# Optimization experiments

Hardware: AMD Instinct MI355X
Metric: run time of the kernel (lower is better)

The kernel has to match this reference:

```python
import math
import jax, jax.numpy as jnp
import numpy as np

ROPE_DIMS = 16  # rope applied to last 16 channels only
N_WIN = 16      # sliding window size


def rmsnorm(x, w):
    return x * jax.lax.rsqrt(jnp.mean(x * x, axis=-1, keepdims=True) + 1e-8) * w


def apply_rope(x, negate=False):
    # x: [B, H, T, C]; rotate last ROPE_DIMS channels with interleaved pairs
    T = x.shape[2]
    x_pass, x_rope = x[..., :-ROPE_DIMS], x[..., -ROPE_DIMS:]
    t = jnp.arange(T, dtype=x.dtype)
    if negate:
        t = -t
    k = jnp.arange(ROPE_DIMS // 2, dtype=x.dtype)
    theta = 10000.0 ** (-2.0 * k / ROPE_DIMS)          # [8]
    freqs = t[:, None] * theta[None, :]                 # [T, 8]
    cos, sin = jnp.cos(freqs), jnp.sin(freqs)
    x1, x2 = x_rope[..., 0::2], x_rope[..., 1::2]
    rx1 = x1 * cos - x2 * sin
    rx2 = x1 * sin + x2 * cos
    rx = jnp.stack([rx1, rx2], axis=-1).reshape(x_rope.shape)
    return jnp.concatenate([x_pass, rx], axis=-1)


def setup_inputs() -> dict:
    key = jax.random.key(0)
    ks = jax.random.split(key, 14)
    B, T, d, c, nh = 4, 2048, 256, 64, 4
    s = 0.02
    return {
        "H": jax.random.normal(ks[0], (B, T, d), jnp.float32),
        "W_Q": jax.random.normal(ks[1], (nh * c, d), jnp.float32) * s,
        "W_K": jax.random.normal(ks[2], (c, d), jnp.float32) * s,
        "W_V": jax.random.normal(ks[3], (c, d), jnp.float32) * s,
        "wq": 1.0 + 0.1 * jax.random.normal(ks[4], (nh, c), jnp.float32),
        "wk": 1.0 + 0.1 * jax.random.normal(ks[5], (c,), jnp.float32),
        "wv": 1.0 + 0.1 * jax.random.normal(ks[6], (c,), jnp.float32),
        "Wg0": jax.random.normal(ks[7], (64, 2 * c), jnp.float32) * s,
        "bg0": jnp.zeros((64,), jnp.float32),
        "Wg1": jax.random.normal(ks[8], (64, 2 * c), jnp.float32) * s,
        "bg1": jnp.zeros((64,), jnp.float32),
        "Wout": jax.random.normal(ks[9], (d, 128), jnp.float32) * s,
        "bout": jnp.zeros((d,), jnp.float32),
    }


def reference(H, W_Q, W_K, W_V, wq, wk, wv, Wg0, bg0, Wg1, bg1, Wout, bout):
    B, T, d = H.shape
    nh, c = wq.shape
    # projections
    Q = (H @ W_Q.T).reshape(B, T, nh, c).transpose(0, 2, 1, 3)   # [B,nh,T,c]
    K = (H @ W_K.T)[:, None]                                      # [B,1,T,c]
    V = (H @ W_V.T)[:, None]                                      # [B,1,T,c]
    # per-head RMSNorm on Q, shared RMSNorm on K/V
    Q = rmsnorm(Q, wq[None, :, None, :])
    K = rmsnorm(K, wk)
    V = rmsnorm(V, wv)
    # partial RoPE (last 16 dims); V is also rotated in this module
    Q = apply_rope(Q)
    K = apply_rope(K)[:, 0]                                       # [B,T,c]
    V = apply_rope(V)[:, 0]
    # dense scores with sliding-window causal mask (width N_WIN)
    S = jnp.einsum('bhtc,bsc->bhts', Q, K) / math.sqrt(c)
    i = jnp.arange(T)[:, None]
    j = jnp.arange(T)[None, :]
    allowed = (j <= i) & (j >= i - (N_WIN - 1))                   # [T,T]
    S = jnp.where(allowed, S, -jnp.inf)
    P = jax.nn.softmax(S, axis=-1)
    O = jnp.einsum('bhts,bsc->bhtc', P, V)                        # [B,nh,T,c]
    O = apply_rope(O, negate=True)
    # group heads {0,1} and {2,3}
    O_g0 = O[:, :2].transpose(0, 2, 1, 3).reshape(B, T, 2 * c)
    O_g1 = O[:, 2:].transpose(0, 2, 1, 3).reshape(B, T, 2 * c)
    p0 = O_g0 @ Wg0.T + bg0
    p1 = O_g1 @ Wg1.T + bg1
    p_all = jnp.concatenate([p0, p1], axis=-1)                    # [B,T,128]
    return p_all @ Wout.T + bout
```

## Files before the change

kernel.cpp:

```cpp
#include <hip/hip_runtime.h>
#include <math.h>

#define T_SEQ 2048
#define DMODEL 256
#define C_HEAD 64
#define NH 4
#define NWIN 16
#define B_SZ 4

typedef __attribute__((ext_vector_type(8))) short bf16x8;
typedef __attribute__((ext_vector_type(8))) unsigned short ushort8;
typedef __attribute__((ext_vector_type(4))) float f32x4;

#define BAR() asm volatile("s_waitcnt lgkmcnt(0)\n\ts_barrier" ::: "memory")

static __device__ __forceinline__ unsigned short f2bf(float f) {
    union { float f; unsigned int u; } v; v.f = f;
    unsigned int r = v.u + 0x7FFFu + ((v.u >> 16) & 1u);
    return (unsigned short)(r >> 16);
}

__global__ __launch_bounds__(256) void conv_w_kernel(
    const float* __restrict__ WQ, const float* __restrict__ WK,
    const float* __restrict__ WV, const float* __restrict__ Wg0,
    const float* __restrict__ Wg1, const float* __restrict__ Wout,
    unsigned short* __restrict__ dst, float2* __restrict__ rtab) {
    const int tid = threadIdx.x;
    if (blockIdx.x >= 72) {
        const int idx = (blockIdx.x - 72) * 256 + tid;
        const int t = idx >> 3, k = idx & 7;
        const float theta = powf(10000.0f, -0.125f * (float)k);
        const float fr = (float)t * theta;
        rtab[idx] = make_float2(cosf(fr), sinf(fr));
        return;
    }
    const int i = blockIdx.x * 256 + tid;
    const float* s; long off; long doff;
    if (i < 12288) {
        const long e = (long)i * 8;
        const int col = (int)(e >> 8), k = (int)(e & 255);
        if      (col < 256) { s = WQ; off = (long)col * 256 + k; }
        else if (col < 320) { s = WK; off = (long)(col - 256) * 256 + k; }
        else                { s = WV; off = (long)(col - 320) * 256 + k; }
        doff = ((long)(col >> 4) * 8 + (k >> 5)) * 512 + ((k >> 3) & 3) * 128 + (col & 15) * 8;
    } else {
        const long e = (long)(i - 12288) * 8;
        const int col = (int)(e >> 7), k = (int)(e & 127);
        if      (col < 64)  { s = Wg0; off = (long)col * 128 + k; }
        else if (col < 128) { s = Wg1; off = (long)(col - 64) * 128 + k; }
        else                { s = Wout; off = (long)(col - 128) * 128 + k; }
        doff = 98304 + ((long)(col >> 4) * 4 + (k >> 5)) * 512 + ((k >> 3) & 3) * 128 + (col & 15) * 8;
    }
    const float4* s4 = (const float4*)(s + off);
    float4 a = s4[0], b = s4[1];
    ushort8 o;
    o[0] = f2bf(a.x); o[1] = f2bf(a.y); o[2] = f2bf(a.z); o[3] = f2bf(a.w);
    o[4] = f2bf(b.x); o[5] = f2bf(b.y); o[6] = f2bf(b.z); o[7] = f2bf(b.w);
    *(ushort8*)(dst + doff) = o;
}

__global__ __launch_bounds__(512) void fused_kernel(
    const float* __restrict__ H, const unsigned short* __restrict__ Wallb,
    const float* __restrict__ wq, const float* __restrict__ wk,
    const float* __restrict__ wv, const float2* __restrict__ rtab,
    const float* __restrict__ bg0, const float* __restrict__ bg1,
    const float* __restrict__ bout, float* __restrict__ out)
{
    __shared__ __align__(16) char smem[37888];
    char* lds_a = smem;
    char* o_lds = smem;
    char* p_lds = smem + 8192;
    char* q_lds = smem + 16384;
    char* k_lds = smem + 24576;
    char* v_t   = smem + 28672;
    char* p_att = smem + 33792;

    const int tid = threadIdx.x;
    const int blk = blockIdx.x;
    const int b  = blk >> 7;
    const int t0 = (blk & 127) << 4;

    const unsigned short* Wpk2 = Wallb + 98304;

    const int w  = tid >> 6;
    const int l  = tid & 63;
    const int g  = l >> 4;
    const int li = l & 15;
    const int lane16 = l * 8;

    const int cb0  = (w < 4) ? (w * 4) : (16 + ((w - 4) >> 1) * 4);
    const int rowa = (w < 4) ? (16 + li) : (((w - 4) & 1) * 16 + li);
    const int sel  = (w - 4) >> 1;
    const int mfh  = (w - 4) & 1;

#define WFRAG(nf, ks) (*(const bf16x8*)(Wallb + (size_t)((cb0 + (nf)) * 8 + (ks)) * 512 + lane16))

    for (int idx = tid; idx < 1024; idx += 512) {
        int row = idx >> 5, ch = idx & 31;
        int t = t0 - 16 + row; if (t < 0) t = 0;
        const float4* s4 = (const float4*)(H + ((size_t)b * T_SEQ + t) * DMODEL + ch * 8);
        float4 a = s4[0], c = s4[1];
        ushort8 o;
        o[0] = f2bf(a.x); o[1] = f2bf(a.y); o[2] = f2bf(a.z); o[3] = f2bf(a.w);
        o[4] = f2bf(c.x); o[5] = f2bf(c.y); o[6] = f2bf(c.z); o[7] = f2bf(c.w);
        int byte = row * 512 + ch * 16;
        byte ^= (row & 7) << 4;
        *(ushort8*)(lds_a + byte) = o;
    }
    bf16x8 cur[4], nxt[4];
    #pragma unroll
    for (int nf = 0; nf < 4; ++nf) { cur[nf] = WFRAG(nf, 0); nxt[nf] = WFRAG(nf, 1); }
    BAR();

    f32x4 acc[4] = {};
    #pragma unroll
    for (int ks = 0; ks < 8; ++ks) {
        bf16x8 fut[4];
        if (ks < 6) {
            #pragma unroll
            for (int nf = 0; nf < 4; ++nf) fut[nf] = WFRAG(nf, ks + 2);
        }
        int abyte = rowa * 512 + (ks * 32 + g * 8) * 2;
        abyte ^= (rowa & 7) << 4;
        bf16x8 a = *(const bf16x8*)(lds_a + abyte);
        #pragma unroll
        for (int nf = 0; nf < 4; ++nf)
            acc[nf] = __builtin_amdgcn_mfma_f32_16x16x32_bf16(a, cur[nf], acc[nf], 0, 0, 0);
        #pragma unroll
        for (int nf = 0; nf < 4; ++nf) { cur[nf] = nxt[nf]; nxt[nf] = fut[nf]; }
    }

    if (w < 4) {
        float gw[4];
        #pragma unroll
        for (int nf = 0; nf < 4; ++nf) gw[nf] = wq[w * 64 + nf * 16 + li];
        #pragma unroll
        for (int r = 0; r < 4; ++r) {
            float x0 = acc[0][r], x1 = acc[1][r];
            float x2 = acc[2][r], x3 = acc[3][r];
            float ss = x0 * x0 + x1 * x1 + x2 * x2 + x3 * x3;
            ss += __shfl_xor(ss, 1);
            ss += __shfl_xor(ss, 2);
            ss += __shfl_xor(ss, 4);
            ss += __shfl_xor(ss, 8);
            const float rinv = rsqrtf(ss * (1.0f / 64.0f) + 1e-8f);
            const int tok = g * 4 + r;
            const int t = t0 + tok;
            float v0 = x0 * rinv * gw[0];
            float v1 = x1 * rinv * gw[1];
            float v2 = x2 * rinv * gw[2];
            float v3 = x3 * rinv * gw[3];
            float2 cs = rtab[t * 8 + (li >> 1)];
            float px = __shfl_xor(v3, 1);
            v3 = ((li & 1) == 0) ? (v3 * cs.x - px * cs.y) : (px * cs.y + v3 * cs.x);
            char* qb = q_lds + w * 2048;
            const int sw = (tok & 7) << 4;
            *(unsigned short*)(qb + ((tok * 128 + (0 * 16 + li) * 2) ^ sw)) = f2bf(v0);
            *(unsigned short*)(qb + ((tok * 128 + (1 * 16 + li) * 2) ^ sw)) = f2bf(v1);
            *(unsigned short*)(qb + ((tok * 128 + (2 * 16 + li) * 2) ^ sw)) = f2bf(v2);
            *(unsigned short*)(qb + ((tok * 128 + (3 * 16 + li) * 2) ^ sw)) = f2bf(v3);
        }
    } else {
        float gw[4];
        #pragma unroll
        for (int nf = 0; nf < 4; ++nf)
            gw[nf] = (sel == 0) ? wk[nf * 16 + li] : wv[nf * 16 + li];
        #pragma unroll
        for (int r = 0; r < 4; ++r) {
            float x0 = acc[0][r], x1 = acc[1][r];
            float x2 = acc[2][r], x3 = acc[3][r];
            float ss = x0 * x0 + x1 * x1 + x2 * x2 + x3 * x3;
            ss += __shfl_xor(ss, 1);
            ss += __shfl_xor(ss, 2);
            ss += __shfl_xor(ss, 4);
            ss += __shfl_xor(ss, 8);
            const float rinv = rsqrtf(ss * (1.0f / 64.0f) + 1e-8f);
            const int row = mfh * 16 + g * 4 + r;
            int tk = t0 - 16 + row; if (tk < 0) tk = 0;
            float v0 = x0 * rinv * gw[0];
            float v1 = x1 * rinv * gw[1];
            float v2 = x2 * rinv * gw[2];
            float v3 = x3 * rinv * gw[3];
            float2 cs = rtab[tk * 8 + (li >> 1)];
            float px = __shfl_xor(v3, 1);
            v3 = ((li & 1) == 0) ? (v3 * cs.x - px * cs.y) : (px * cs.y + v3 * cs.x);
            if (sel == 0) {
                const int sw = (row & 7) << 4;
                *(unsigned short*)(k_lds + ((row * 128 + (0 * 16 + li) * 2) ^ sw)) = f2bf(v0);
                *(unsigned short*)(k_lds + ((row * 128 + (1 * 16 + li) * 2) ^ sw)) = f2bf(v1);
                *(unsigned short*)(k_lds + ((row * 128 + (2 * 16 + li) * 2) ^ sw)) = f2bf(v2);
                *(unsigned short*)(k_lds + ((row * 128 + (3 * 16 + li) * 2) ^ sw)) = f2bf(v3);
            } else {
                *(unsigned short*)(v_t + (0 * 16 + li) * 80 + row * 2) = f2bf(v0);
                *(unsigned short*)(v_t + (1 * 16 + li) * 80 + row * 2) = f2bf(v1);
                *(unsigned short*)(v_t + (2 * 16 + li) * 80 + row * 2) = f2bf(v2);
                *(unsigned short*)(v_t + (3 * 16 + li) * 80 + row * 2) = f2bf(v3);
            }
        }
    }
    BAR();

    const int gate = w >> 2, colq = w & 3;
    bf16x8 gpre[4];
    if (w >= 4) {
        #pragma unroll
        for (int ks = 0; ks < 4; ++ks)
            gpre[ks] = *(const bf16x8*)(Wpk2 + (size_t)((gate * 4 + colq) * 4 + ks) * 512 + lane16);
    }
    if (w < 4) {
        const int h = w;
        bf16x8 qf0, qf1;
        {
            const char* qb = q_lds + h * 2048;
            const int sw = (li & 7) << 4;
            qf0 = *(const bf16x8*)(qb + ((li * 128 + g * 16) ^ sw));
            qf1 = *(const bf16x8*)(qb + ((li * 128 + 64 + g * 16) ^ sw));
        }
        f32x4 st[2];
        #pragma unroll
        for (int tile = 0; tile < 2; ++tile) {
            const int row = tile * 16 + li;
            const int sw = (row & 7) << 4;
            bf16x8 kf0 = *(const bf16x8*)(k_lds + ((row * 128 + g * 16) ^ sw));
            bf16x8 kf1 = *(const bf16x8*)(k_lds + ((row * 128 + 64 + g * 16) ^ sw));
            f32x4 sa = {};
            sa = __builtin_amdgcn_mfma_f32_16x16x32_bf16(kf0, qf0, sa, 0, 0, 0);
            sa = __builtin_amdgcn_mfma_f32_16x16x32_bf16(kf1, qf1, sa, 0, 0, 0);
            st[tile] = sa;
        }

        float p[8];
        float mx = -1e30f;
        #pragma unroll
        for (int tile = 0; tile < 2; ++tile) {
            #pragma unroll
            for (int r = 0; r < 4; ++r) {
                int krel = tile * 16 - 16 + g * 4 + r;
                int dd = li - krel;
                bool ok = ((unsigned)dd < 16u) && (t0 + krel >= 0);
                float v = ok ? st[tile][r] * 0.125f : -1e30f;
                p[tile * 4 + r] = v;
                mx = fmaxf(mx, v);
            }
        }
        mx = fmaxf(mx, __shfl_xor(mx, 16));
        mx = fmaxf(mx, __shfl_xor(mx, 32));
        float sum = 0.f;
        #pragma unroll
        for (int i = 0; i < 8; ++i) { p[i] = __expf(p[i] - mx); sum += p[i]; }
        sum += __shfl_xor(sum, 16);
        sum += __shfl_xor(sum, 32);
        const float inv = 1.0f / sum;

        bf16x8 paf;
        {
            char* pbase = p_att + h * 1024;
            uint2 w0, w1;
            w0.x = (unsigned)f2bf(p[0] * inv) | ((unsigned)f2bf(p[1] * inv) << 16);
            w0.y = (unsigned)f2bf(p[2] * inv) | ((unsigned)f2bf(p[3] * inv) << 16);
            w1.x = (unsigned)f2bf(p[4] * inv) | ((unsigned)f2bf(p[5] * inv) << 16);
            w1.y = (unsigned)f2bf(p[6] * inv) | ((unsigned)f2bf(p[7] * inv) << 16);
            const int sw = (li & 3) << 4;
            *(uint2*)(pbase + ((li * 64 + 0 * 32 + g * 8) ^ sw)) = w0;
            *(uint2*)(pbase + ((li * 64 + 1 * 32 + g * 8) ^ sw)) = w1;
            asm volatile("s_waitcnt lgkmcnt(0)" ::: "memory");
            paf = *(const bf16x8*)(pbase + ((li * 64 + g * 16) ^ sw));
        }

        f32x4 o[4] = {};
        #pragma unroll
        for (int ctile = 0; ctile < 4; ++ctile) {
            bf16x8 vf = *(const bf16x8*)(v_t + (ctile * 16 + li) * 80 + g * 16);
            o[ctile] = __builtin_amdgcn_mfma_f32_16x16x32_bf16(paf, vf, o[ctile], 0, 0, 0);
        }

        #pragma unroll
        for (int r = 0; r < 4; ++r) {
            const int row = g * 4 + r;
            const int t = t0 + row;
            float o3 = o[3][r];
            float po = __shfl_xor(o3, 1);
            float2 cs = rtab[t * 8 + (li >> 1)];
            o3 = ((li & 1) == 0) ? (o3 * cs.x + po * cs.y) : (-po * cs.y + o3 * cs.x);
            #pragma unroll
            for (int ctile = 0; ctile < 4; ++ctile) {
                const int col = h * 64 + ctile * 16 + li;
                int byte = row * 512 + col * 2;
                byte ^= (row & 7) << 4;
                float val = (ctile == 3) ? o3 : o[ctile][r];
                *(unsigned short*)(o_lds + byte) = f2bf(val);
            }
        }
        #pragma unroll
        for (int ks = 0; ks < 4; ++ks)
            gpre[ks] = *(const bf16x8*)(Wpk2 + (size_t)((gate * 4 + colq) * 4 + ks) * 512 + lane16);
    }
    BAR();

    bf16x8 opre[2][4];
    {
        const float* bg = gate ? bg1 : bg0;
        f32x4 accp = {};
        #pragma unroll
        for (int ks = 0; ks < 4; ++ks) {
            int byte = li * 512 + (gate * 128 + ks * 32 + g * 8) * 2;
            byte ^= (li & 7) << 4;
            bf16x8 a = *(const bf16x8*)(o_lds + byte);
            accp = __builtin_amdgcn_mfma_f32_16x16x32_bf16(a, gpre[ks], accp, 0, 0, 0);
        }
        #pragma unroll
        for (int nf = 0; nf < 2; ++nf)
            #pragma unroll
            for (int ks = 0; ks < 4; ++ks)
                opre[nf][ks] = *(const bf16x8*)(Wpk2 + (size_t)((8 + w * 2 + nf) * 4 + ks) * 512 + lane16);
        const int cl = colq * 16 + li;
        const int pcol = gate * 64 + cl;
        const float bb = bg[cl];
        #pragma unroll
        for (int r = 0; r < 4; ++r) {
            const int row = g * 4 + r;
            int byte = row * 256 + pcol * 2;
            byte ^= (row & 7) << 4;
            *(unsigned short*)(p_lds + byte) = f2bf(accp[r] + bb);
        }
    }
    BAR();

    {
        f32x4 acco[2] = {};
        #pragma unroll
        for (int ks = 0; ks < 4; ++ks) {
            int byte = li * 256 + (ks * 32 + g * 8) * 2;
            byte ^= (li & 7) << 4;
            bf16x8 a = *(const bf16x8*)(p_lds + byte);
            #pragma unroll
            for (int nf = 0; nf < 2; ++nf)
                acco[nf] = __builtin_amdgcn_mfma_f32_16x16x32_bf16(a, opre[nf][ks], acco[nf], 0, 0, 0);
        }
        #pragma unroll
        for (int nf = 0; nf < 2; ++nf) {
            const int col = w * 32 + nf * 16 + li;
            const float bb = bout[col];
            #pragma unroll
            for (int r = 0; r < 4; ++r) {
                const int row = g * 4 + r;
                out[(size_t)(b * T_SEQ + t0 + row) * DMODEL + col] = acco[nf][r] + bb;
            }
        }
    }
#undef WFRAG
}

extern "C" void kernel_launch(void* const* d_in, const int* in_sizes, int n_in,
                              void* d_out, int out_size, void* d_ws, size_t ws_size,
                              hipStream_t stream) {
    const float* H    = (const float*)d_in[0];
    const float* WQ   = (const float*)d_in[1];
    const float* WK   = (const float*)d_in[2];
    const float* WV   = (const float*)d_in[3];
    const float* wq   = (const float*)d_in[4];
    const float* wk   = (const float*)d_in[5];
    const float* wv   = (const float*)d_in[6];
    const float* Wg0  = (const float*)d_in[7];
    const float* bg0  = (const float*)d_in[8];
    const float* Wg1  = (const float*)d_in[9];
    const float* bg1  = (const float*)d_in[10];
    const float* Wout = (const float*)d_in[11];
    const float* bout = (const float*)d_in[12];
    float* out = (float*)d_out;

    char* ws = (char*)d_ws;
    unsigned short* Wallb = (unsigned short*)ws;
    float2* rtab = (float2*)(ws + 294912);

    conv_w_kernel<<<136, 256, 0, stream>>>(WQ, WK, WV, Wg0, Wg1, Wout, Wallb, rtab);
    fused_kernel<<<B_SZ * T_SEQ / 16, 512, 0, stream>>>(H, Wallb, wq, wk, wv, rtab,
                                                        bg0, bg1, bout, out);
}
```

Baseline: 22.38 us.

## Run fused attention block as a single wavefront, removing barriers and H staging

Each 16-token block now runs on one 64-thread wavefront instead of eight waves. That wave holds H in registers as bf16 fragments instead of staging it in LDS, and loops serially over the K/V, Q-head, attention, gate and output projections. Cross-wave barriers become plain LDS waitcnt fences, and RoPE cos/sin values are loaded once into registers. The theta powf is also replaced by a constant table. This removes barrier and LDS staging costs, but each block now has an 8x longer serial chain and much less parallelism inside a CU. Only 512 waves cover the whole GPU, so latency hiding is at risk.

Measured after the change: 87.16 us. 289% more time.

```diff
diff --git a/kernel.cpp b/kernel.cpp
--- a/kernel.cpp
+++ b/kernel.cpp
@@ -12,7 +12,8 @@
 typedef __attribute__((ext_vector_type(8))) unsigned short ushort8;
 typedef __attribute__((ext_vector_type(4))) float f32x4;
 
-#define BAR() asm volatile("s_waitcnt lgkmcnt(0)\n\ts_barrier" ::: "memory")
+#define MFMA(a, b, c) __builtin_amdgcn_mfma_f32_16x16x32_bf16(a, b, c, 0, 0, 0)
+#define FENCE() asm volatile("s_waitcnt lgkmcnt(0)" ::: "memory")
 
 static __device__ __forceinline__ unsigned short f2bf(float f) {
     union { float f; unsigned int u; } v; v.f = f;
@@ -27,10 +28,13 @@
     unsigned short* __restrict__ dst, float2* __restrict__ rtab) {
     const int tid = threadIdx.x;
     if (blockIdx.x >= 72) {
+        const float th_tab[8] = {1.f, 0.31622776601683794f, 0.1f,
+                                 0.03162277660168379f, 0.01f,
+                                 0.0031622776601683794f, 0.001f,
+                                 0.00031622776601683794f};
         const int idx = (blockIdx.x - 72) * 256 + tid;
         const int t = idx >> 3, k = idx & 7;
-        const float theta = powf(10000.0f, -0.125f * (float)k);
-        const float fr = (float)t * theta;
+        const float fr = (float)t * th_tab[k];
         rtab[idx] = make_float2(cosf(fr), sinf(fr));
         return;
     }
@@ -59,81 +63,130 @@
     *(ushort8*)(dst + doff) = o;
 }
 
-__global__ __launch_bounds__(512) void fused_kernel(
+__global__ __launch_bounds__(64) void fused_kernel(
     const float* __restrict__ H, const unsigned short* __restrict__ Wallb,
     const float* __restrict__ wq, const float* __restrict__ wk,
     const float* __restrict__ wv, const float2* __restrict__ rtab,
     const float* __restrict__ bg0, const float* __restrict__ bg1,
     const float* __restrict__ bout, float* __restrict__ out)
 {
-    __shared__ __align__(16) char smem[37888];
-    char* lds_a = smem;
-    char* o_lds = smem;
-    char* p_lds = smem + 8192;
-    char* q_lds = smem + 16384;
-    char* k_lds = smem + 24576;
-    char* v_t   = smem + 28672;
-    char* p_att = smem + 33792;
-
-    const int tid = threadIdx.x;
+    __shared__ __align__(16) char smem[30720];
+    char* q_lds = smem;
+    char* k_lds = smem + 8192;
+    char* v_t   = smem + 12288;
+    char* p_att = smem + 17408;
+    char* o_lds = smem + 18432;
+    char* p_lds = smem + 26624;
+
+    const int l   = threadIdx.x;
     const int blk = blockIdx.x;
-    const int b  = blk >> 7;
-    const int t0 = (blk & 127) << 4;
-
+    const int b   = blk >> 7;
+    const int t0  = (blk & 127) << 4;
+    const int g   = l >> 4;
+    const int li  = l & 15;
+    const int lane16 = l * 8;
     const unsigned short* Wpk2 = Wallb + 98304;
 
-    const int w  = tid >> 6;
-    const int l  = tid & 63;
-    const int g  = l >> 4;
-    const int li = l & 15;
-    const int lane16 = l * 8;
-
-    const int cb0  = (w < 4) ? (w * 4) : (16 + ((w - 4) >> 1) * 4);
-    const int rowa = (w < 4) ? (16 + li) : (((w - 4) & 1) * 16 + li);
-    const int sel  = (w - 4) >> 1;
-    const int mfh  = (w - 4) & 1;
-
-#define WFRAG(nf, ks) (*(const bf16x8*)(Wallb + (size_t)((cb0 + (nf)) * 8 + (ks)) * 512 + lane16))
-
-    for (int idx = tid; idx < 1024; idx += 512) {
-        int row = idx >> 5, ch = idx & 31;
-        int t = t0 - 16 + row; if (t < 0) t = 0;
-        const float4* s4 = (const float4*)(H + ((size_t)b * T_SEQ + t) * DMODEL + ch * 8);
-        float4 a = s4[0], c = s4[1];
-        ushort8 o;
-        o[0] = f2bf(a.x); o[1] = f2bf(a.y); o[2] = f2bf(a.z); o[3] = f2bf(a.w);
-        o[4] = f2bf(c.x); o[5] = f2bf(c.y); o[6] = f2bf(c.z); o[7] = f2bf(c.w);
-        int byte = row * 512 + ch * 16;
-        byte ^= (row & 7) << 4;
-        *(ushort8*)(lds_a + byte) = o;
-    }
-    bf16x8 cur[4], nxt[4];
-    #pragma unroll
-    for (int nf = 0; nf < 4; ++nf) { cur[nf] = WFRAG(nf, 0); nxt[nf] = WFRAG(nf, 1); }
-    BAR();
-
-    f32x4 acc[4] = {};
-    #pragma unroll
-    for (int ks = 0; ks < 8; ++ks) {
-        bf16x8 fut[4];
-        if (ks < 6) {
-            #pragma unroll
-            for (int nf = 0; nf < 4; ++nf) fut[nf] = WFRAG(nf, ks + 2);
-        }
-        int abyte = rowa * 512 + (ks * 32 + g * 8) * 2;
-        abyte ^= (rowa & 7) << 4;
-        bf16x8 a = *(const bf16x8*)(lds_a + abyte);
+    float2 csT[4], csH[4];
+    #pragma unroll
+    for (int r = 0; r < 4; ++r) {
+        csT[r] = rtab[(t0 + g * 4 + r) * 8 + (li >> 1)];
+        int tk = t0 - 16 + g * 4 + r; if (tk < 0) tk = 0;
+        csH[r] = rtab[tk * 8 + (li >> 1)];
+    }
+
+    bf16x8 hA0[8], hA1[8];
+    {
+        int r0 = t0 - 16 + li; if (r0 < 0) r0 = 0;
+        const float* p0 = H + ((size_t)b * T_SEQ + r0) * DMODEL + g * 8;
+        const float* p1 = H + ((size_t)b * T_SEQ + t0 + li) * DMODEL + g * 8;
+        #pragma unroll
+        for (int ks = 0; ks < 8; ++ks) {
+            float4 a0 = *(const float4*)(p0 + ks * 32);
+            float4 c0 = *(const float4*)(p0 + ks * 32 + 4);
+            float4 a1 = *(const float4*)(p1 + ks * 32);
+            float4 c1 = *(const float4*)(p1 + ks * 32 + 4);
+            bf16x8 t0v, t1v;
+            t0v[0] = (short)f2bf(a0.x); t0v[1] = (short)f2bf(a0.y);
+            t0v[2] = (short)f2bf(a0.z); t0v[3] = (short)f2bf(a0.w);
+            t0v[4] = (short)f2bf(c0.x); t0v[5] = (short)f2bf(c0.y);
+            t0v[6] = (short)f2bf(c0.z); t0v[7] = (short)f2bf(c0.w);
+            t1v[0] = (short)f2bf(a1.x); t1v[1] = (short)f2bf(a1.y);
+            t1v[2] = (short)f2bf(a1.z); t1v[3] = (short)f2bf(a1.w);
+            t1v[4] = (short)f2bf(c1.x); t1v[5] = (short)f2bf(c1.y);
+            t1v[6] = (short)f2bf(c1.z); t1v[7] = (short)f2bf(c1.w);
+            hA0[ks] = t0v;
+            hA1[ks] = t1v;
+        }
+    }
+
+    #pragma unroll
+    for (int sel = 0; sel < 2; ++sel) {
+        f32x4 acc[2][4] = {};
+        #pragma unroll
+        for (int ks = 0; ks < 8; ++ks) {
+            #pragma unroll
+            for (int nf = 0; nf < 4; ++nf) {
+                bf16x8 wf = *(const bf16x8*)(Wallb + (size_t)((16 + sel * 4 + nf) * 8 + ks) * 512 + lane16);
+                acc[0][nf] = MFMA(hA0[ks], wf, acc[0][nf]);
+                acc[1][nf] = MFMA(hA1[ks], wf, acc[1][nf]);
+            }
+        }
+        float gw[4];
         #pragma unroll
         for (int nf = 0; nf < 4; ++nf)
-            acc[nf] = __builtin_amdgcn_mfma_f32_16x16x32_bf16(a, cur[nf], acc[nf], 0, 0, 0);
-        #pragma unroll
-        for (int nf = 0; nf < 4; ++nf) { cur[nf] = nxt[nf]; nxt[nf] = fut[nf]; }
-    }
-
-    if (w < 4) {
+            gw[nf] = (sel == 0) ? wk[nf * 16 + li] : wv[nf * 16 + li];
+        #pragma unroll
+        for (int tt = 0; tt < 2; ++tt) {
+            #pragma unroll
+            for (int r = 0; r < 4; ++r) {
+                float x0 = acc[tt][0][r], x1 = acc[tt][1][r];
+                float x2 = acc[tt][2][r], x3 = acc[tt][3][r];
+                float ss = x0 * x0 + x1 * x1 + x2 * x2 + x3 * x3;
+                ss += __shfl_xor(ss, 1);
+                ss += __shfl_xor(ss, 2);
+                ss += __shfl_xor(ss, 4);
+                ss += __shfl_xor(ss, 8);
+                const float rinv = rsqrtf(ss * (1.0f / 64.0f) + 1e-8f);
+                const int row = tt * 16 + g * 4 + r;
+                float v0 = x0 * rinv * gw[0];
+                float v1 = x1 * rinv * gw[1];
+                float v2 = x2 * rinv * gw[2];
+                float v3 = x3 * rinv * gw[3];
+                float2 cs = tt ? csT[r] : csH[r];
+                float px = __shfl_xor(v3, 1);
+                v3 = ((li & 1) == 0) ? (v3 * cs.x - px * cs.y) : (px * cs.y + v3 * cs.x);
+                if (sel == 0) {
+                    const int sw = (row & 7) << 4;
+                    *(unsigned short*)(k_lds + ((row * 128 + (0 * 16 + li) * 2) ^ sw)) = f2bf(v0);
+                    *(unsigned short*)(k_lds + ((row * 128 + (1 * 16 + li) * 2) ^ sw)) = f2bf(v1);
+                    *(unsigned short*)(k_lds + ((row * 128 + (2 * 16 + li) * 2) ^ sw)) = f2bf(v2);
+                    *(unsigned short*)(k_lds + ((row * 128 + (3 * 16 + li) * 2) ^ sw)) = f2bf(v3);
+                } else {
+                    *(unsigned short*)(v_t + (0 * 16 + li) * 80 + row * 2) = f2bf(v0);
+                    *(unsigned short*)(v_t + (1 * 16 + li) * 80 + row * 2) = f2bf(v1);
+                    *(unsigned short*)(v_t + (2 * 16 + li) * 80 + row * 2) = f2bf(v2);
+                    *(unsigned short*)(v_t + (3 * 16 + li) * 80 + row * 2) = f2bf(v3);
+                }
+            }
+        }
+    }
+
+    #pragma unroll
+    for (int hh = 0; hh < 4; ++hh) {
+        f32x4 acc[4] = {};
+        #pragma unroll
+        for (int ks = 0; ks < 8; ++ks) {
+            #pragma unroll
+            for (int nf = 0; nf < 4; ++nf) {
+                bf16x8 wf = *(const bf16x8*)(Wallb + (size_t)((hh * 4 + nf) * 8 + ks) * 512 + lane16);
+                acc[nf] = MFMA(hA1[ks], wf, acc[nf]);
+            }
+        }
         float gw[4];
         #pragma unroll
-        for (int nf = 0; nf < 4; ++nf) gw[nf] = wq[w * 64 + nf * 16 + li];
+        for (int nf = 0; nf < 4; ++nf) gw[nf] = wq[hh * 64 + nf * 16 + li];
+        char* qb = q_lds + hh * 2048;
         #pragma unroll
         for (int r = 0; r < 4; ++r) {
             float x0 = acc[0][r], x1 = acc[1][r];
@@ -145,87 +198,46 @@
             ss += __shfl_xor(ss, 8);
             const float rinv = rsqrtf(ss * (1.0f / 64.0f) + 1e-8f);
             const int tok = g * 4 + r;
-            const int t = t0 + tok;
             float v0 = x0 * rinv * gw[0];
             float v1 = x1 * rinv * gw[1];
             float v2 = x2 * rinv * gw[2];
             float v3 = x3 * rinv * gw[3];
-            float2 cs = rtab[t * 8 + (li >> 1)];
+            float2 cs = csT[r];
             float px = __shfl_xor(v3, 1);
             v3 = ((li & 1) == 0) ? (v3 * cs.x - px * cs.y) : (px * cs.y + v3 * cs.x);
-            char* qb = q_lds + w * 2048;
             const int sw = (tok & 7) << 4;
             *(unsigned short*)(qb + ((tok * 128 + (0 * 16 + li) * 2) ^ sw)) = f2bf(v0);
             *(unsigned short*)(qb + ((tok * 128 + (1 * 16 + li) * 2) ^ sw)) = f2bf(v1);
             *(unsigned short*)(qb + ((tok * 128 + (2 * 16 + li) * 2) ^ sw)) = f2bf(v2);
             *(unsigned short*)(qb + ((tok * 128 + (3 * 16 + li) * 2) ^ sw)) = f2bf(v3);
         }
-    } else {
-        float gw[4];
-        #pragma unroll
-        for (int nf = 0; nf < 4; ++nf)
-            gw[nf] = (sel == 0) ? wk[nf * 16 + li] : wv[nf * 16 + li];
-        #pragma unroll
-        for (int r = 0; r < 4; ++r) {
-            float x0 = acc[0][r], x1 = acc[1][r];
-            float x2 = acc[2][r], x3 = acc[3][r];
-            float ss = x0 * x0 + x1 * x1 + x2 * x2 + x3 * x3;
-            ss += __shfl_xor(ss, 1);
-            ss += __shfl_xor(ss, 2);
-            ss += __shfl_xor(ss, 4);
-            ss += __shfl_xor(ss, 8);
-            const float rinv = rsqrtf(ss * (1.0f / 64.0f) + 1e-8f);
-            const int row = mfh * 16 + g * 4 + r;
-            int tk = t0 - 16 + row; if (tk < 0) tk = 0;
-            float v0 = x0 * rinv * gw[0];
-            float v1 = x1 * rinv * gw[1];
-            float v2 = x2 * rinv * gw[2];
-            float v3 = x3 * rinv * gw[3];
-            float2 cs = rtab[tk * 8 + (li >> 1)];
-            float px = __shfl_xor(v3, 1);
-            v3 = ((li & 1) == 0) ? (v3 * cs.x - px * cs.y) : (px * cs.y + v3 * cs.x);
-            if (sel == 0) {
-                const int sw = (row & 7) << 4;
-                *(unsigned short*)(k_lds + ((row * 128 + (0 * 16 + li) * 2) ^ sw)) = f2bf(v0);
-                *(unsigned short*)(k_lds + ((row * 128 + (1 * 16 + li) * 2) ^ sw)) = f2bf(v1);
-                *(unsigned short*)(k_lds + ((row * 128 + (2 * 16 + li) * 2) ^ sw)) = f2bf(v2);
-                *(unsigned short*)(k_lds + ((row * 128 + (3 * 16 + li) * 2) ^ sw)) = f2bf(v3);
-            } else {
-                *(unsigned short*)(v_t + (0 * 16 + li) * 80 + row * 2) = f2bf(v0);
-                *(unsigned short*)(v_t + (1 * 16 + li) * 80 + row * 2) = f2bf(v1);
-                *(unsigned short*)(v_t + (2 * 16 + li) * 80 + row * 2) = f2bf(v2);
-                *(unsigned short*)(v_t + (3 * 16 + li) * 80 + row * 2) = f2bf(v3);
-            }
-        }
-    }
-    BAR();
-
-    const int gate = w >> 2, colq = w & 3;
-    bf16x8 gpre[4];
-    if (w >= 4) {
-        #pragma unroll
-        for (int ks = 0; ks < 4; ++ks)
-            gpre[ks] = *(const bf16x8*)(Wpk2 + (size_t)((gate * 4 + colq) * 4 + ks) * 512 + lane16);
-    }
-    if (w < 4) {
-        const int h = w;
-        bf16x8 qf0, qf1;
-        {
-            const char* qb = q_lds + h * 2048;
-            const int sw = (li & 7) << 4;
-            qf0 = *(const bf16x8*)(qb + ((li * 128 + g * 16) ^ sw));
-            qf1 = *(const bf16x8*)(qb + ((li * 128 + 64 + g * 16) ^ sw));
-        }
+    }
+    FENCE();
+
+    bf16x8 kf[2][2], vf[4];
+    #pragma unroll
+    for (int tile = 0; tile < 2; ++tile) {
+        const int row = tile * 16 + li;
+        const int sw = (row & 7) << 4;
+        kf[tile][0] = *(const bf16x8*)(k_lds + ((row * 128 + g * 16) ^ sw));
+        kf[tile][1] = *(const bf16x8*)(k_lds + ((row * 128 + 64 + g * 16) ^ sw));
+    }
+    #pragma unroll
+    for (int ct = 0; ct < 4; ++ct)
+        vf[ct] = *(const bf16x8*)(v_t + (ct * 16 + li) * 80 + g * 16);
+
+    #pragma unroll
+    for (int hh = 0; hh < 4; ++hh) {
+        const char* qb = q_lds + hh * 2048;
+        const int swq = (li & 7) << 4;
+        bf16x8 qf0 = *(const bf16x8*)(qb + ((li * 128 + g * 16) ^ swq));
+        bf16x8 qf1 = *(const bf16x8*)(qb + ((li * 128 + 64 + g * 16) ^ swq));
         f32x4 st[2];
         #pragma unroll
         for (int tile = 0; tile < 2; ++tile) {
-            const int row = tile * 16 + li;
-            const int sw = (row & 7) << 4;
-            bf16x8 kf0 = *(const bf16x8*)(k_lds + ((row * 128 + g * 16) ^ sw));
-            bf16x8 kf1 = *(const bf16x8*)(k_lds + ((row * 128 + 64 + g * 16) ^ sw));
             f32x4 sa = {};
-            sa = __builtin_amdgcn_mfma_f32_16x16x32_bf16(kf0, qf0, sa, 0, 0, 0);
-            sa = __builtin_amdgcn_mfma_f32_16x16x32_bf16(kf1, qf1, sa, 0, 0, 0);
+            sa = MFMA(kf[tile][0], qf0, sa);
+            sa = MFMA(kf[tile][1], qf1, sa);
             st[tile] = sa;
         }
 
@@ -254,68 +266,57 @@
 
         bf16x8 paf;
         {
-            char* pbase = p_att + h * 1024;
             uint2 w0, w1;
             w0.x = (unsigned)f2bf(p[0] * inv) | ((unsigned)f2bf(p[1] * inv) << 16);
             w0.y = (unsigned)f2bf(p[2] * inv) | ((unsigned)f2bf(p[3] * inv) << 16);
             w1.x = (unsigned)f2bf(p[4] * inv) | ((unsigned)f2bf(p[5] * inv) << 16);
             w1.y = (unsigned)f2bf(p[6] * inv) | ((unsigned)f2bf(p[7] * inv) << 16);
             const int sw = (li & 3) << 4;
-            *(uint2*)(pbase + ((li * 64 + 0 * 32 + g * 8) ^ sw)) = w0;
-            *(uint2*)(pbase + ((li * 64 + 1 * 32 + g * 8) ^ sw)) = w1;
-            asm volatile("s_waitcnt lgkmcnt(0)" ::: "memory");
-            paf = *(const bf16x8*)(pbase + ((li * 64 + g * 16) ^ sw));
+            *(uint2*)(p_att + ((li * 64 + 0 * 32 + g * 8) ^ sw)) = w0;
+            *(uint2*)(p_att + ((li * 64 + 1 * 32 + g * 8) ^ sw)) = w1;
+            FENCE();
+            paf = *(const bf16x8*)(p_att + ((li * 64 + g * 16) ^ sw));
         }
 
         f32x4 o[4] = {};
         #pragma unroll
-        for (int ctile = 0; ctile < 4; ++ctile) {
-            bf16x8 vf = *(const bf16x8*)(v_t + (ctile * 16 + li) * 80 + g * 16);
-            o[ctile] = __builtin_amdgcn_mfma_f32_16x16x32_bf16(paf, vf, o[ctile], 0, 0, 0);
-        }
+        for (int ct = 0; ct < 4; ++ct)
+            o[ct] = MFMA(paf, vf[ct], o[ct]);
 
         #pragma unroll
         for (int r = 0; r < 4; ++r) {
             const int row = g * 4 + r;
-            const int t = t0 + row;
             float o3 = o[3][r];
             float po = __shfl_xor(o3, 1);
-            float2 cs = rtab[t * 8 + (li >> 1)];
+            float2 cs = csT[r];
             o3 = ((li & 1) == 0) ? (o3 * cs.x + po * cs.y) : (-po * cs.y + o3 * cs.x);
             #pragma unroll
-            for (int ctile = 0; ctile < 4; ++ctile) {
-                const int col = h * 64 + ctile * 16 + li;
+            for (int ct = 0; ct < 4; ++ct) {
+                const int col = hh * 64 + ct * 16 + li;
                 int byte = row * 512 + col * 2;
                 byte ^= (row & 7) << 4;
-                float val = (ctile == 3) ? o3 : o[ctile][r];
+                float val = (ct == 3) ? o3 : o[ct][r];
                 *(unsigned short*)(o_lds + byte) = f2bf(val);
             }
         }
-        #pragma unroll
-        for (int ks = 0; ks < 4; ++ks)
-            gpre[ks] = *(const bf16x8*)(Wpk2 + (size_t)((gate * 4 + colq) * 4 + ks) * 512 + lane16);
-    }
-    BAR();
-
-    bf16x8 opre[2][4];
-    {
-        const float* bg = gate ? bg1 : bg0;
+    }
+    FENCE();
+
+    #pragma unroll
+    for (int cq = 0; cq < 8; ++cq) {
+        const int gate = cq >> 2;
         f32x4 accp = {};
         #pragma unroll
         for (int ks = 0; ks < 4; ++ks) {
             int byte = li * 512 + (gate * 128 + ks * 32 + g * 8) * 2;
             byte ^= (li & 7) << 4;
             bf16x8 a = *(const bf16x8*)(o_lds + byte);
-            accp = __builtin_amdgcn_mfma_f32_16x16x32_bf16(a, gpre[ks], accp, 0, 0, 0);
-        }
-        #pragma unroll
-        for (int nf = 0; nf < 2; ++nf)
-            #pragma unroll
-            for (int ks = 0; ks < 4; ++ks)
-                opre[nf][ks] = *(const bf16x8*)(Wpk2 + (size_t)((8 + w * 2 + nf) * 4 + ks) * 512 + lane16);
-        const int cl = colq * 16 + li;
+            bf16x8 wf = *(const bf16x8*)(Wpk2 + (size_t)(cq * 4 + ks) * 512 + lane16);
+            accp = MFMA(a, wf, accp);
+        }
+        const int cl = (cq & 3) * 16 + li;
         const int pcol = gate * 64 + cl;
-        const float bb = bg[cl];
+        const float bb = gate ? bg1[cl] : bg0[cl];
         #pragma unroll
         for (int r = 0; r < 4; ++r) {
             const int row = g * 4 + r;
@@ -324,31 +325,27 @@
             *(unsigned short*)(p_lds + byte) = f2bf(accp[r] + bb);
         }
     }
-    BAR();
-
-    {
-        f32x4 acco[2] = {};
+    FENCE();
+
+    #pragma unroll
+    for (int cb = 0; cb < 16; ++cb) {
+        f32x4 acco = {};
         #pragma unroll
         for (int ks = 0; ks < 4; ++ks) {
             int byte = li * 256 + (ks * 32 + g * 8) * 2;
             byte ^= (li & 7) << 4;
             bf16x8 a = *(const bf16x8*)(p_lds + byte);
-            #pragma unroll
-            for (int nf = 0; nf < 2; ++nf)
-                acco[nf] = __builtin_amdgcn_mfma_f32_16x16x32_bf16(a, opre[nf][ks], acco[nf], 0, 0, 0);
-        }
-        #pragma unroll
-        for (int nf = 0; nf < 2; ++nf) {
-            const int col = w * 32 + nf * 16 + li;
-            const float bb = bout[col];
-            #pragma unroll
-            for (int r = 0; r < 4; ++r) {
-                const int row = g * 4 + r;
-                out[(size_t)(b * T_SEQ + t0 + row) * DMODEL + col] = acco[nf][r] + bb;
-            }
-        }
-    }
-#undef WFRAG
+            bf16x8 wf = *(const bf16x8*)(Wpk2 + (size_t)((8 + cb) * 4 + ks) * 512 + lane16);
+            acco = MFMA(a, wf, acco);
+        }
+        const int col = cb * 16 + li;
+        const float bb = bout[col];
+        #pragma unroll
+        for (int r = 0; r < 4; ++r) {
+            const int row = g * 4 + r;
+            out[(size_t)(b * T_SEQ + t0 + row) * DMODEL + col] = acco[r] + bb;
+        }
+    }
 }
 
 extern "C" void kernel_launch(void* const* d_in, const int* in_sizes, int n_in,
@@ -374,6 +371,6 @@
     float2* rtab = (float2*)(ws + 294912);
 
     conv_w_kernel<<<136, 256, 0, stream>>>(WQ, WK, WV, Wg0, Wg1, Wout, Wallb, rtab);
-    fused_kernel<<<B_SZ * T_SEQ / 16, 512, 0, stream>>>(H, Wallb, wq, wk, wv, rtab,
-                                                        bg0, bg1, bout, out);
+    fused_kernel<<<B_SZ * T_SEQ / 16, 64, 0, stream>>>(H, Wallb, wq, wk, wv, rtab,
+                                                       bg0, bg1, bout, out);
 }
```
